# Optimization experiments

Hardware: AMD Instinct MI355X
Metric: run time of the kernel (lower is better)

## Reference

```python
import jax, jax.numpy as jnp
import numpy as np

T, D, H, HD = 2048, 2048, 16, 128
ROPE_BASE = 10000.0
NEG = jnp.float32(-1e30)


def rms_norm(x):
    # F.rms_norm(x, (x.size(-1),)) with default eps = dtype eps
    eps = jnp.finfo(x.dtype).eps
    return x * jax.lax.rsqrt(jnp.mean(x * x, axis=-1, keepdims=True) + eps)


def rotary(x):
    # x: [1, T, H, hd]; half-split rotation as in Rotary.forward
    hd = x.shape[-1]
    inv_freq = (1.0 / ROPE_BASE) ** (jnp.arange(0, hd, 2, dtype=jnp.float32) / hd)
    t = jnp.arange(x.shape[1], dtype=jnp.float32)
    freqs = jnp.outer(t, inv_freq)                      # [T, hd/2]
    cos = jnp.cos(freqs)[None, :, None, :]
    sin = jnp.sin(freqs)[None, :, None, :]
    x1, x2 = jnp.split(x, 2, axis=-1)
    return jnp.concatenate([x1 * cos + x2 * sin, -x1 * sin + x2 * cos], axis=-1)


def setup_inputs() -> dict:
    key = jax.random.key(0)
    ks = jax.random.split(key, 10)
    w = lambda k, shape: jax.random.normal(k, shape, jnp.float32) * 0.02
    return {
        "x":  jax.random.normal(ks[0], (1, T, D), jnp.float32),
        "vi": jax.random.normal(ks[1], (1, T, H, HD), jnp.float32),
        "x0": jax.random.normal(ks[2], (1, T, D), jnp.float32),
        "wq": w(ks[3], (D, D)),
        "wk": w(ks[4], (D, D)),
        "wv": w(ks[5], (D, D)),
        "wo": w(ks[6], (D, D)),
        "lamb": jnp.float32(0.5),
        "lambdas": jnp.array([1.0, 0.0], jnp.float32),
        "w_fc": w(ks[7], (4 * D, D)),
        "w_proj": w(ks[8], (D, 4 * D)),
    }


def reference(x, vi, x0, wq, wk, wv, wo, lamb, lambdas, w_fc, w_proj):
    # Block: residual blend with initial embedding x0
    xb = lambdas[0] * x + lambdas[1] * x0
    xn = rms_norm(xb)

    # --- CausalSelfAttention ---
    q = (xn @ wq.T).reshape(1, T, H, HD)
    k = (xn @ wk.T).reshape(1, T, H, HD)
    v = (xn @ wv.T).reshape(1, T, H, HD)
    v = (1.0 - lamb) * v + lamb * vi                     # value-embedding blend
    q = rotary(rms_norm(q))
    k = rotary(rms_norm(k))

    scale = 1.0 / jnp.sqrt(jnp.float32(HD))              # flex_attention default scale
    scores = jnp.einsum('bqhd,bkhd->bhqk', q, k) * scale # [1,H,T,T]
    causal = jnp.tril(jnp.ones((T, T), bool))
    scores = jnp.where(causal[None, None], scores, NEG)
    attn = jax.nn.softmax(scores, axis=-1)
    y = jnp.einsum('bhqk,bkhd->bqhd', attn, v).reshape(1, T, D)
    a = y @ wo.T                                         # attention output REPLACES x (no residual)

    # --- MLP with squared ReLU ---
    h = rms_norm(a) @ w_fc.T
    h = jnp.square(jax.nn.relu(h))
    out = a + h @ w_proj.T
    return out
```

## Files before the change

### kernel.cpp

```cpp
#include <hip/hip_runtime.h>
#include <hip/hip_bf16.h>

typedef __bf16 bf16;
typedef __bf16 bf16x8 __attribute__((ext_vector_type(8)));
typedef float f32x4 __attribute__((ext_vector_type(4)));
typedef unsigned int u32x4 __attribute__((ext_vector_type(4)));

#define DD 2048
#define DD2 4194304ull
#define G9_LDS 131072

__device__ __forceinline__ void glds16(const void* g, void* l) {
  __builtin_amdgcn_global_load_lds((const __attribute__((address_space(1))) void*)g,
                                   (__attribute__((address_space(3))) void*)l, 16, 0, 0);
}

__device__ __forceinline__ f32x4 mfma16(bf16x8 a, bf16x8 b, f32x4 c) {
  return __builtin_amdgcn_mfma_f32_16x16x32_bf16(a, b, c, 0, 0, 0);
}

__device__ __forceinline__ unsigned pk2(float lo, float hi) {
  unsigned short a = __builtin_bit_cast(unsigned short, (bf16)lo);
  unsigned short b = __builtin_bit_cast(unsigned short, (bf16)hi);
  return (unsigned)a | ((unsigned)b << 16);
}

__global__ __launch_bounds__(256) void cvt_seg(const float* __restrict__ s0, const float* __restrict__ s1,
                                               const float* __restrict__ s2, const float* __restrict__ s3,
                                               bf16* __restrict__ dst, int seglog, size_t total) {
  size_t i = ((size_t)blockIdx.x * 256 + threadIdx.x) * 16;
  const size_t stride = (size_t)gridDim.x * 256 * 16;
  for (; i < total; i += stride) {
    int seg = (int)(i >> seglog);
    const float* src = (seg == 0) ? s0 : (seg == 1) ? s1 : (seg == 2) ? s2 : s3;
    size_t loc = i - ((size_t)seg << seglog);
    float4 a0 = *(const float4*)(src + loc);
    float4 a1 = *(const float4*)(src + loc + 4);
    float4 a2 = *(const float4*)(src + loc + 8);
    float4 a3 = *(const float4*)(src + loc + 12);
    bf16x8 o0, o1;
    o0[0] = (bf16)a0.x; o0[1] = (bf16)a0.y; o0[2] = (bf16)a0.z; o0[3] = (bf16)a0.w;
    o0[4] = (bf16)a1.x; o0[5] = (bf16)a1.y; o0[6] = (bf16)a1.z; o0[7] = (bf16)a1.w;
    o1[0] = (bf16)a2.x; o1[1] = (bf16)a2.y; o1[2] = (bf16)a2.z; o1[3] = (bf16)a2.w;
    o1[4] = (bf16)a3.x; o1[5] = (bf16)a3.y; o1[6] = (bf16)a3.z; o1[7] = (bf16)a3.w;
    *(bf16x8*)(dst + i) = o0;
    *(bf16x8*)(dst + i + 8) = o1;
  }
}

template<bool BLEND>
__global__ __launch_bounds__(256) void prenorm_k(const float* __restrict__ x, const float* __restrict__ x0,
                                                 const float* __restrict__ lambdas, bf16* __restrict__ out) {
  const int t = blockIdx.x, tid = threadIdx.x;
  const float4* xr = (const float4*)(x + (size_t)t * DD);
  float4 a0 = xr[2 * tid], a1 = xr[2 * tid + 1];
  float v[8] = {a0.x, a0.y, a0.z, a0.w, a1.x, a1.y, a1.z, a1.w};
  if (BLEND) {
    const float l0 = lambdas[0], l1 = lambdas[1];
    const float4* yr = (const float4*)(x0 + (size_t)t * DD);
    float4 b0 = yr[2 * tid], b1 = yr[2 * tid + 1];
    float w[8] = {b0.x, b0.y, b0.z, b0.w, b1.x, b1.y, b1.z, b1.w};
#pragma unroll
    for (int i = 0; i < 8; ++i) v[i] = l0 * v[i] + l1 * w[i];
  }
  float ss = 0.f;
#pragma unroll
  for (int i = 0; i < 8; ++i) ss += v[i] * v[i];
#pragma unroll
  for (int off = 1; off < 64; off <<= 1) ss += __shfl_xor(ss, off, 64);
  __shared__ float red[4];
  const int wid = tid >> 6;
  if ((tid & 63) == 0) red[wid] = ss;
  __syncthreads();
  ss = red[0] + red[1] + red[2] + red[3];
  const float sc = rsqrtf(ss * (1.0f / DD) + 1.1920928955078125e-07f);
  bf16x8 o;
#pragma unroll
  for (int i = 0; i < 8; ++i) o[i] = (bf16)(v[i] * sc);
  *(bf16x8*)(out + (size_t)t * DD + tid * 8) = o;
}

__global__ __launch_bounds__(256) void rope_k(bf16* __restrict__ qg, bf16* __restrict__ kg) {
  const int tid = threadIdx.x, lane = tid & 63, wid = tid >> 6;
  const int p = blockIdx.x * 4 + wid;
  bf16* base = ((p >> 15) ? kg : qg);
  const int t = (p >> 4) & 2047, hh = p & 15;
  base += (size_t)t * DD + hh * 128;
  float x1 = (float)base[lane], x2 = (float)base[lane + 64];
  float ss = x1 * x1 + x2 * x2;
#pragma unroll
  for (int off = 1; off < 64; off <<= 1) ss += __shfl_xor(ss, off, 64);
  const float sc = rsqrtf(ss * (1.0f / 128.0f) + 1.1920928955078125e-07f);
  x1 *= sc; x2 *= sc;
  const float fr = (float)t * exp2f((float)lane * (-13.287712379549449f / 64.0f));
  const float s = sinf(fr), c = cosf(fr);
  base[lane]      = (bf16)(x1 * c + x2 * s);
  base[lane + 64] = (bf16)(-x1 * s + x2 * c);
}

__global__ __launch_bounds__(256) void vt_k(const bf16* __restrict__ v, bf16* __restrict__ vt) {
  __shared__ alignas(16) bf16 tile[16 * 128];
  const int tb = blockIdx.x, hb = blockIdx.y, tid = threadIdx.x;
  glds16(v + (size_t)(tb * 16 + (tid >> 4)) * DD + hb * 128 + (tid & 15) * 8, tile + tid * 8);
  __syncthreads();
  const int d_l = tid & 127, tc = tid >> 7;
  bf16x8 o;
#pragma unroll
  for (int i = 0; i < 8; ++i) o[i] = tile[(tc * 8 + i) * 128 + d_l];
  *(bf16x8*)(vt + (size_t)(hb * 128 + d_l) * DD + tb * 16 + tc * 8) = o;
}

__device__ __forceinline__ void g9_stageA(const bf16* A, int Kstride, int row0, int k0,
                                          bf16* buf, int hm, int tid) {
#pragma unroll
  for (int i = 0; i < 2; ++i) {
    int e = tid + i * 512;
    int prl = e >> 3, slot = e & 7;
    int wm = prl >> 6, r63 = prl & 63;
    glds16(A + (size_t)(row0 + wm * 128 + hm * 64 + r63) * Kstride + k0 + ((slot ^ (prl & 7)) * 8),
           buf + hm * 8192 + e * 8);
  }
}
__device__ __forceinline__ void g9_stageB(const bf16* B, int Kstride, int col0, int k0,
                                          bf16* buf, int hn, int tid) {
#pragma unroll
  for (int i = 0; i < 2; ++i) {
    int e = tid + i * 512;
    int pbl = e >> 3, slot = e & 7;
    int wn = pbl >> 5, q = pbl & 31;
    glds16(B + (size_t)(col0 + wn * 64 + hn * 32 + q) * Kstride + k0 + ((slot ^ (pbl & 7)) * 8),
           buf + 16384 + hn * 8192 + e * 8);
  }
}

__device__ __forceinline__ void gemm9_core(const bf16* __restrict__ A, const bf16* __restrict__ B,
                                           int Kstride, int Klen, int row0, int col0,
                                           bf16* smem, f32x4 (&acc)[8][4]) {
  const int tid = threadIdx.x, lane = tid & 63, wid = tid >> 6;
  const int wm = wid >> 2, wn = wid & 3;
  const int l15 = lane & 15, g = lane >> 4;
  const int sw = l15 & 7;
  const int NT = Klen >> 6;
  g9_stageA(A, Kstride, row0, 0, smem, 0, tid);
  g9_stageB(B, Kstride, col0, 0, smem, 0, tid);
  g9_stageB(B, Kstride, col0, 0, smem, 1, tid);
  g9_stageA(A, Kstride, row0, 0, smem, 1, tid);
  asm volatile("s_waitcnt vmcnt(4)" ::: "memory");
  __builtin_amdgcn_s_barrier();

  bf16x8 a[4][2], b0[2][2], b1[2][2];
  for (int t = 0; t < NT; ++t) {
    bf16* cb = smem + (t & 1) * 32768;
    bf16* sb = smem + ((t + 1) & 1) * 32768;
    const int ks0 = (t + 1) << 6;
    const bool st = (t + 1) < NT;
#pragma unroll
    for (int mm = 0; mm < 4; ++mm)
#pragma unroll
      for (int ks = 0; ks < 2; ++ks)
        a[mm][ks] = *(const bf16x8*)(cb + (wm * 64 + mm * 16 + l15) * 64 + (((ks * 4 + g) ^ sw) * 8));
#pragma unroll
    for (int nn = 0; nn < 2; ++nn)
#pragma unroll
      for (int ks = 0; ks < 2; ++ks)
        b0[nn][ks] = *(const bf16x8*)(cb + 16384 + (wn * 32 + nn * 16 + l15) * 64 + (((ks * 4 + g) ^ sw) * 8));
    if (st) g9_stageA(A, Kstride, row0, ks0, sb, 0, tid);
    if (st) { asm volatile("s_waitcnt vmcnt(4)" ::: "memory"); }
    else    { asm volatile("s_waitcnt vmcnt(2)" ::: "memory"); }
    __builtin_amdgcn_s_barrier();
    __builtin_amdgcn_s_setprio(1);
#pragma unroll
    for (int mm = 0; mm < 4; ++mm)
#pragma unroll
      for (int nn = 0; nn < 2; ++nn)
#pragma unroll
        for (int ks = 0; ks < 2; ++ks)
          acc[mm][nn] = mfma16(a[mm][ks], b0[nn][ks], acc[mm][nn]);
    __builtin_amdgcn_s_setprio(0);
#pragma unroll
    for (int nn = 0; nn < 2; ++nn)
#pragma unroll
      for (int ks = 0; ks < 2; ++ks)
        b1[nn][ks] = *(const bf16x8*)(cb + 16384 + 8192 + (wn * 32 + nn * 16 + l15) * 64 + (((ks * 4 + g) ^ sw) * 8));
    if (st) g9_stageB(B, Kstride, col0, ks0, sb, 0, tid);
    if (st) { asm volatile("s_waitcnt vmcnt(4)" ::: "memory"); }
    else    { asm volatile("s_waitcnt vmcnt(0)" ::: "memory"); }
    __builtin_amdgcn_s_barrier();
    __builtin_amdgcn_s_setprio(1);
#pragma unroll
    for (int mm = 0; mm < 4; ++mm)
#pragma unroll
      for (int nn = 0; nn < 2; ++nn)
#pragma unroll
        for (int ks = 0; ks < 2; ++ks)
          acc[mm][2 + nn] = mfma16(a[mm][ks], b1[nn][ks], acc[mm][2 + nn]);
    __builtin_amdgcn_s_setprio(0);
#pragma unroll
    for (int mm = 0; mm < 4; ++mm)
#pragma unroll
      for (int ks = 0; ks < 2; ++ks)
        a[mm][ks] = *(const bf16x8*)(cb + 8192 + (wm * 64 + mm * 16 + l15) * 64 + (((ks * 4 + g) ^ sw) * 8));
    if (st) g9_stageB(B, Kstride, col0, ks0, sb, 1, tid);
    __builtin_amdgcn_s_barrier();
    __builtin_amdgcn_s_setprio(1);
#pragma unroll
    for (int mm = 0; mm < 4; ++mm)
#pragma unroll
      for (int nn = 0; nn < 2; ++nn)
#pragma unroll
        for (int ks = 0; ks < 2; ++ks)
          acc[4 + mm][nn] = mfma16(a[mm][ks], b0[nn][ks], acc[4 + mm][nn]);
    __builtin_amdgcn_s_setprio(0);
    if (st) { g9_stageA(A, Kstride, row0, ks0, sb, 1, tid);
              asm volatile("s_waitcnt vmcnt(4)" ::: "memory"); }
    __builtin_amdgcn_s_barrier();
    __builtin_amdgcn_s_setprio(1);
#pragma unroll
    for (int mm = 0; mm < 4; ++mm)
#pragma unroll
      for (int nn = 0; nn < 2; ++nn)
#pragma unroll
        for (int ks = 0; ks < 2; ++ks)
          acc[4 + mm][2 + nn] = mfma16(a[mm][ks], b1[nn][ks], acc[4 + mm][2 + nn]);
    __builtin_amdgcn_s_setprio(0);
  }
}

#define GEMM9_EPI(STMT)                                                        \
  { const int lane_ = threadIdx.x & 63, wid_ = threadIdx.x >> 6;               \
    const int l15_ = lane_ & 15, g_ = lane_ >> 4;                              \
    const int wm_ = wid_ >> 2, wn_ = wid_ & 3;                                 \
    _Pragma("unroll") for (int m = 0; m < 8; ++m)                              \
    _Pragma("unroll") for (int n = 0; n < 4; ++n)                              \
    _Pragma("unroll") for (int j = 0; j < 4; ++j) {                            \
      int grow = row0 + wm_ * 128 + (m >> 2) * 64 + (m & 3) * 16 + g_ * 4 + j; \
      int gcol = col0 + wn_ * 64 + (n >> 1) * 32 + (n & 1) * 16 + l15_;        \
      float vacc = acc[m][n][j];                                               \
      STMT; } }

__global__ __launch_bounds__(512, 1) void gemm9_qkv(const bf16* __restrict__ A,
    const bf16* __restrict__ Wq, const bf16* __restrict__ Wk, const bf16* __restrict__ Wv,
    bf16* __restrict__ oq, bf16* __restrict__ ok, bf16* __restrict__ ov,
    const float* __restrict__ vi, const float* __restrict__ lambp) {
  extern __shared__ bf16 smem9[];
  const int z = blockIdx.z;
  const bf16* B = (z == 0) ? Wq : (z == 1) ? Wk : Wv;
  bf16* out = (z == 0) ? oq : (z == 1) ? ok : ov;
  const int row0 = blockIdx.y * 256, col0 = blockIdx.x * 256;
  f32x4 acc[8][4] = {};
  gemm9_core(A, B, DD, DD, row0, col0, smem9, acc);
  if (z < 2) {
    GEMM9_EPI( out[(size_t)grow * DD + gcol] = (bf16)vacc; )
  } else {
    const float lam = *lambp;
    GEMM9_EPI( out[(size_t)grow * DD + gcol] =
                 (bf16)((1.0f - lam) * vacc + lam * vi[(size_t)grow * DD + gcol]); )
  }
}

__global__ __launch_bounds__(512, 1) void gemm9_part(const bf16* __restrict__ A, const bf16* __restrict__ B,
                                                     float* __restrict__ o1, float* __restrict__ o2,
                                                     int zsw, int N, int Kstride, int Klen) {
  extern __shared__ bf16 smem9[];
  const int row0 = blockIdx.y * 256, col0 = blockIdx.x * 256;
  const int z = blockIdx.z, kofs = z * Klen;
  float* out = (z < zsw) ? (o1 + (size_t)z * DD2) : (o2 + (size_t)(z - zsw) * DD2);
  f32x4 acc[8][4] = {};
  gemm9_core(A + kofs, B + kofs, Kstride, Klen, row0, col0, smem9, acc);
  GEMM9_EPI( out[(size_t)grow * N + gcol] = vacc; )
}

__global__ __launch_bounds__(512, 1) void gemm9_relu(const bf16* __restrict__ A, const bf16* __restrict__ B,
                                                     bf16* __restrict__ out, int N, int Kstride, int Klen) {
  extern __shared__ bf16 smem9[];
  const int row0 = blockIdx.y * 256, col0 = blockIdx.x * 256;
  f32x4 acc[8][4] = {};
  gemm9_core(A, B, Kstride, Klen, row0, col0, smem9, acc);
  GEMM9_EPI( float r = fmaxf(vacc, 0.f); out[(size_t)grow * N + gcol] = (bf16)(r * r); )
}

__global__ __launch_bounds__(256) void wo_red_prenorm(const float* __restrict__ pa, const float* __restrict__ pb,
                                                      float* __restrict__ a_f, bf16* __restrict__ an) {
  const int t = blockIdx.x, tid = threadIdx.x;
  const size_t base = (size_t)t * DD + tid * 8;
  float v[8];
#pragma unroll
  for (int h = 0; h < 2; ++h) {
    size_t i = base + h * 4;
    float4 r0 = *(const float4*)(pa + i);
    float4 r1 = *(const float4*)(pa + DD2 + i);
    float4 r2 = *(const float4*)(pb + i);
    float4 r3 = *(const float4*)(pb + DD2 + i);
    v[h*4+0] = r0.x + r1.x + r2.x + r3.x;
    v[h*4+1] = r0.y + r1.y + r2.y + r3.y;
    v[h*4+2] = r0.z + r1.z + r2.z + r3.z;
    v[h*4+3] = r0.w + r1.w + r2.w + r3.w;
  }
  *(float4*)(a_f + base)     = make_float4(v[0], v[1], v[2], v[3]);
  *(float4*)(a_f + base + 4) = make_float4(v[4], v[5], v[6], v[7]);
  float ss = 0.f;
#pragma unroll
  for (int i = 0; i < 8; ++i) ss += v[i] * v[i];
#pragma unroll
  for (int off = 1; off < 64; off <<= 1) ss += __shfl_xor(ss, off, 64);
  __shared__ float red[4];
  if ((tid & 63) == 0) red[tid >> 6] = ss;
  __syncthreads();
  ss = red[0] + red[1] + red[2] + red[3];
  const float sc = rsqrtf(ss * (1.0f / DD) + 1.1920928955078125e-07f);
  bf16x8 o;
#pragma unroll
  for (int i = 0; i < 8; ++i) o[i] = (bf16)(v[i] * sc);
  *(bf16x8*)(an + base) = o;
}

__global__ __launch_bounds__(256) void proj_red(const float* __restrict__ pa, const float* __restrict__ pw,
                                                const float* __restrict__ a_f, float* __restrict__ out) {
  const size_t base = ((size_t)blockIdx.x * 256 + threadIdx.x) * 8;
#pragma unroll
  for (int h = 0; h < 2; ++h) {
    size_t i = base + h * 4;
    float4 r = *(const float4*)(a_f + i);
    float4 u = *(const float4*)(pa + i);
    float4 w = *(const float4*)(pa + DD2 + i);
    float4 z = *(const float4*)(pa + 2 * DD2 + i);
    float4 y = *(const float4*)(pw + i);
    *(float4*)(out + i) = make_float4(r.x + u.x + w.x + z.x + y.x,
                                      r.y + u.y + w.y + z.y + y.y,
                                      r.z + u.z + w.z + z.z + y.z,
                                      r.w + u.w + w.w + z.w + y.w);
  }
}

__device__ __forceinline__ void att_stageK(const bf16* kg, int h, int kt, bf16* dst, int tid) {
#pragma unroll
  for (int r = 0; r < 2; ++r) {
    int e = tid + r * 256, row = e >> 4, slot = e & 15;
    glds16(kg + (size_t)(kt * 32 + row) * DD + h * 128 + ((slot ^ (row & 7)) * 8), dst + e * 8);
  }
}
__device__ __forceinline__ void att_stageV(const bf16* vtg, int h, int kt, bf16* dst, int tid) {
#pragma unroll
  for (int r = 0; r < 2; ++r) {
    int e = tid + r * 256, d = e >> 2, slot = e & 3;
    glds16(vtg + (size_t)(h * 128 + d) * DD + kt * 32 + ((slot ^ ((d >> 1) & 3)) * 8), dst + e * 8);
  }
}

__global__ __launch_bounds__(256) void attn_k(const bf16* __restrict__ qg, const bf16* __restrict__ kg,
                                              const bf16* __restrict__ vtg, bf16* __restrict__ yg) {
  __shared__ alignas(16) bf16 Ks[3][32 * 128];
  __shared__ alignas(16) bf16 Vt[3][128 * 32];
  const int h = blockIdx.y, qb = 31 - blockIdx.x;
  const int tid = threadIdx.x, lane = tid & 63, wid = tid >> 6;
  const int l15 = lane & 15, g = lane >> 4, swl = l15 & 7;
  const int qrow = qb * 64 + wid * 16;
  const float scale = 0.08838834764831845f;
  bf16x8 aQ[4];
  {
    const bf16* qp = qg + (size_t)(qrow + l15) * DD + h * 128 + g * 8;
#pragma unroll
    for (int kc = 0; kc < 4; ++kc) aQ[kc] = *(const bf16x8*)(qp + kc * 32);
  }
  f32x4 acc[8] = {};
  float lsum = 0.f;
  const int nkt = qb * 2 + 2;
  att_stageK(kg, h, 0, Ks[0], tid);
  att_stageV(vtg, h, 0, Vt[0], tid);
  att_stageK(kg, h, 1, Ks[1], tid);
  att_stageV(vtg, h, 1, Vt[1], tid);
  asm volatile("s_waitcnt vmcnt(4)" ::: "memory");
  __builtin_amdgcn_s_barrier();
  int cur = 0;
  for (int kt = 0; kt < nkt; ++kt) {
    const int kbase = kt * 32;
    const int nb = (cur >= 1) ? cur - 1 : 2;
    bf16x8 kf0[4], kf1[4];
#pragma unroll
    for (int kc = 0; kc < 4; ++kc) {
      kf0[kc] = *(const bf16x8*)(Ks[cur] + l15 * 128 + (((kc * 4 + g) ^ swl) * 8));
      kf1[kc] = *(const bf16x8*)(Ks[cur] + (16 + l15) * 128 + (((kc * 4 + g) ^ swl) * 8));
    }
    if (kt + 2 < nkt) { att_stageK(kg, h, kt + 2, Ks[nb], tid);
                        att_stageV(vtg, h, kt + 2, Vt[nb], tid); }
    f32x4 S0 = {}, S1 = {};
#pragma unroll
    for (int kc = 0; kc < 4; ++kc) {
      S0 = mfma16(kf0[kc], aQ[kc], S0);
      S1 = mfma16(kf1[kc], aQ[kc], S1);
    }
    const int q = qrow + l15;
    float p0[4], p1[4];
#pragma unroll
    for (int j = 0; j < 4; ++j) {
      int k0 = kbase + 4 * g + j;
      p0[j] = (k0 <= q) ? __expf(S0[j] * scale) : 0.f;
      p1[j] = (k0 + 16 <= q) ? __expf(S1[j] * scale) : 0.f;
      lsum += p0[j] + p1[j];
    }
    unsigned w0 = pk2(p0[0], p0[1]), w1 = pk2(p0[2], p0[3]);
    unsigned w2 = pk2(p1[0], p1[1]), w3 = pk2(p1[2], p1[3]);
    const int s0l = (g & 1) * 32 + l15, s1l = s0l + 16;
    const bool hi = g >= 2;
    unsigned t00 = __shfl(w0, s0l, 64), t10 = __shfl(w1, s0l, 64);
    unsigned t01 = __shfl(w0, s1l, 64), t11 = __shfl(w1, s1l, 64);
    unsigned u00 = __shfl(w2, s0l, 64), u10 = __shfl(w3, s0l, 64);
    unsigned u01 = __shfl(w2, s1l, 64), u11 = __shfl(w3, s1l, 64);
    u32x4 av = { hi ? u00 : t00, hi ? u10 : t10, hi ? u01 : t01, hi ? u11 : t11 };
    bf16x8 aP = __builtin_bit_cast(bf16x8, av);
#pragma unroll
    for (int dt = 0; dt < 8; ++dt) {
      int d = dt * 16 + l15;
      bf16x8 bV = *(const bf16x8*)(Vt[cur] + d * 32 + ((g ^ ((d >> 1) & 3)) * 8));
      acc[dt] = mfma16(aP, bV, acc[dt]);
    }
    if (kt + 1 < nkt) {
      if (kt + 2 < nkt) { asm volatile("s_waitcnt vmcnt(4)" ::: "memory"); }
      else              { asm volatile("s_waitcnt vmcnt(0)" ::: "memory"); }
      __builtin_amdgcn_s_barrier();
    }
    cur = (cur == 2) ? 0 : cur + 1;
  }
  lsum += __shfl_xor(lsum, 16, 64);
  lsum += __shfl_xor(lsum, 32, 64);
  f32x4 linv;
#pragma unroll
  for (int j = 0; j < 4; ++j) linv[j] = 1.0f / __shfl(lsum, 4 * g + j, 64);
#pragma unroll
  for (int dt = 0; dt < 8; ++dt)
#pragma unroll
    for (int j = 0; j < 4; ++j) {
      int q = qrow + 4 * g + j;
      yg[(size_t)q * DD + h * 128 + dt * 16 + l15] = (bf16)(acc[dt][j] * linv[j]);
    }
}

extern "C" void kernel_launch(void* const* d_in, const int* in_sizes, int n_in,
                              void* d_out, int out_size, void* d_ws, size_t ws_size,
                              hipStream_t stream) {
  const float* x       = (const float*)d_in[0];
  const float* vi      = (const float*)d_in[1];
  const float* x0      = (const float*)d_in[2];
  const float* wq      = (const float*)d_in[3];
  const float* wk      = (const float*)d_in[4];
  const float* wv      = (const float*)d_in[5];
  const float* wo      = (const float*)d_in[6];
  const float* lamb    = (const float*)d_in[7];
  const float* lambdas = (const float*)d_in[8];
  const float* wfc     = (const float*)d_in[9];
  const float* wproj   = (const float*)d_in[10];
  float* out = (float*)d_out;

  (void)hipFuncSetAttribute(reinterpret_cast<const void*>(gemm9_qkv),
                            hipFuncAttributeMaxDynamicSharedMemorySize, G9_LDS);
  (void)hipFuncSetAttribute(reinterpret_cast<const void*>(gemm9_part),
                            hipFuncAttributeMaxDynamicSharedMemorySize, G9_LDS);
  (void)hipFuncSetAttribute(reinterpret_cast<const void*>(gemm9_relu),
                            hipFuncAttributeMaxDynamicSharedMemorySize, G9_LDS);

  char* wsb = (char*)d_ws;
  size_t off = 0;
  auto alloc = [&](size_t bytes) { void* p = wsb + off; off = (off + bytes + 255) & ~(size_t)255; return p; };
  bf16* wq_b  = (bf16*)alloc(DD2 * 2);
  bf16* wk_b  = (bf16*)alloc(DD2 * 2);
  bf16* wv_b  = (bf16*)alloc(DD2 * 2);
  bf16* wo_b  = (bf16*)alloc(DD2 * 2);
  bf16* wfc_b = (bf16*)alloc(DD2 * 8);
  bf16* wpj_b = (bf16*)alloc(DD2 * 8);
  bf16* xn_b  = (bf16*)alloc(DD2 * 2);
  bf16* q_b   = (bf16*)alloc(DD2 * 2);
  bf16* k_b   = (bf16*)alloc(DD2 * 2);
  bf16* v_b   = (bf16*)alloc(DD2 * 2);
  bf16* y_b   = (bf16*)alloc(DD2 * 2);
  bf16* an_b  = (bf16*)alloc(DD2 * 2);
  float* partA = (float*)xn_b;
  float* a_f  = (float*)alloc(DD2 * 4);
  bf16* h_b   = (bf16*)alloc(DD2 * 8);
  bf16* vt_b  = h_b;
  float* partB = (float*)h_b;

  cvt_seg<<<2048, 256, 0, stream>>>(wq, wk, wv, wo, (bf16*)wsb, 22, 4 * DD2);
  prenorm_k<true><<<2048, 256, 0, stream>>>(x, x0, lambdas, xn_b);
  gemm9_qkv<<<dim3(8, 8, 3), 512, G9_LDS, stream>>>(xn_b, wq_b, wk_b, wv_b, q_b, k_b, v_b, vi, lamb);
  rope_k<<<16384, 256, 0, stream>>>(q_b, k_b);
  vt_k<<<dim3(128, 16), 256, 0, stream>>>(v_b, vt_b);
  attn_k<<<dim3(32, 16), 256, 0, stream>>>(q_b, k_b, vt_b, y_b);
  gemm9_part<<<dim3(8, 8, 4), 512, G9_LDS, stream>>>(y_b, wo_b, partA, partB, 2, DD, DD, 512);
  wo_red_prenorm<<<2048, 256, 0, stream>>>(partA, partB, a_f, an_b);
  cvt_seg<<<2048, 256, 0, stream>>>(wfc, wproj, wfc, wfc, wfc_b, 24, 8 * DD2);
  gemm9_relu<<<dim3(32, 8), 512, G9_LDS, stream>>>(an_b, wfc_b, h_b, 4 * DD, DD, DD);
  gemm9_part<<<dim3(8, 8, 4), 512, G9_LDS, stream>>>(h_b, wpj_b, partA, (float*)wfc_b, 3, DD, 4 * DD, 2048);
  proj_red<<<2048, 256, 0, stream>>>(partA, (float*)wfc_b, a_f, out);
}
```

Before: 386.0 us.

## Shrink GEMM tiles to 128x128 and halve split-K partitions

Replaces the 256x256-tile GEMM core (128 KB LDS, one block per CU) with a 128x128-tile core using 64 KB LDS and launch bounds allowing several blocks per CU. Grids grow accordingly, and split-K for the output and projection GEMMs drops from four partitions to two, so the reduction kernels read fewer partial buffers. The aim is more resident blocks and less partial-sum traffic. The cost is lower arithmetic intensity per tile, more global and LDS traffic per FLOP, and longer K loops per block.

After: 387.5 us. Within noise of the previous version (+0.4%).

```diff
diff --git a/kernel.cpp b/kernel.cpp
--- a/kernel.cpp
+++ b/kernel.cpp
@@ -8,7 +8,7 @@
 
 #define DD 2048
 #define DD2 4194304ull
-#define G9_LDS 131072
+#define G10_LDS 65536
 
 __device__ __forceinline__ void glds16(const void* g, void* l) {
   __builtin_amdgcn_global_load_lds((const __attribute__((address_space(1))) void*)g,
@@ -110,176 +110,162 @@
   *(bf16x8*)(vt + (size_t)(hb * 128 + d_l) * DD + tb * 16 + tc * 8) = o;
 }
 
-__device__ __forceinline__ void g9_stageA(const bf16* A, int Kstride, int row0, int k0,
-                                          bf16* buf, int hm, int tid) {
-#pragma unroll
-  for (int i = 0; i < 2; ++i) {
-    int e = tid + i * 512;
-    int prl = e >> 3, slot = e & 7;
-    int wm = prl >> 6, r63 = prl & 63;
-    glds16(A + (size_t)(row0 + wm * 128 + hm * 64 + r63) * Kstride + k0 + ((slot ^ (prl & 7)) * 8),
-           buf + hm * 8192 + e * 8);
-  }
-}
-__device__ __forceinline__ void g9_stageB(const bf16* B, int Kstride, int col0, int k0,
-                                          bf16* buf, int hn, int tid) {
-#pragma unroll
-  for (int i = 0; i < 2; ++i) {
-    int e = tid + i * 512;
-    int pbl = e >> 3, slot = e & 7;
-    int wn = pbl >> 5, q = pbl & 31;
-    glds16(B + (size_t)(col0 + wn * 64 + hn * 32 + q) * Kstride + k0 + ((slot ^ (pbl & 7)) * 8),
-           buf + 16384 + hn * 8192 + e * 8);
-  }
-}
-
-__device__ __forceinline__ void gemm9_core(const bf16* __restrict__ A, const bf16* __restrict__ B,
-                                           int Kstride, int Klen, int row0, int col0,
-                                           bf16* smem, f32x4 (&acc)[8][4]) {
+__device__ __forceinline__ void g10_stageA(const bf16* A, int Kstride, int row0, int k0,
+                                           bf16* buf, int hm, int tid) {
+  int prl = tid >> 3, slot = tid & 7;
+  int wmb = prl >> 5, r31 = prl & 31;
+  glds16(A + (size_t)(row0 + wmb * 64 + hm * 32 + r31) * Kstride + k0 + ((slot ^ (prl & 7)) * 8),
+         buf + hm * 4096 + tid * 8);
+}
+__device__ __forceinline__ void g10_stageB(const bf16* B, int Kstride, int col0, int k0,
+                                           bf16* buf, int hn, int tid) {
+  int pbl = tid >> 3, slot = tid & 7;
+  int wnb = pbl >> 4, c15 = pbl & 15;
+  glds16(B + (size_t)(col0 + wnb * 32 + hn * 16 + c15) * Kstride + k0 + ((slot ^ (pbl & 7)) * 8),
+         buf + 8192 + hn * 4096 + tid * 8);
+}
+
+__device__ __forceinline__ void gemm10_core(const bf16* __restrict__ A, const bf16* __restrict__ B,
+                                            int Kstride, int Klen, int row0, int col0,
+                                            bf16* smem, f32x4 (&acc)[4][2]) {
   const int tid = threadIdx.x, lane = tid & 63, wid = tid >> 6;
   const int wm = wid >> 2, wn = wid & 3;
   const int l15 = lane & 15, g = lane >> 4;
-  const int sw = l15 & 7;
   const int NT = Klen >> 6;
-  g9_stageA(A, Kstride, row0, 0, smem, 0, tid);
-  g9_stageB(B, Kstride, col0, 0, smem, 0, tid);
-  g9_stageB(B, Kstride, col0, 0, smem, 1, tid);
-  g9_stageA(A, Kstride, row0, 0, smem, 1, tid);
-  asm volatile("s_waitcnt vmcnt(4)" ::: "memory");
+  g10_stageA(A, Kstride, row0, 0, smem, 0, tid);
+  g10_stageB(B, Kstride, col0, 0, smem, 0, tid);
+  g10_stageB(B, Kstride, col0, 0, smem, 1, tid);
+  g10_stageA(A, Kstride, row0, 0, smem, 1, tid);
+  asm volatile("s_waitcnt vmcnt(2)" ::: "memory");
   __builtin_amdgcn_s_barrier();
 
-  bf16x8 a[4][2], b0[2][2], b1[2][2];
+  bf16x8 a[2][2], b0[2], b1[2];
   for (int t = 0; t < NT; ++t) {
-    bf16* cb = smem + (t & 1) * 32768;
-    bf16* sb = smem + ((t + 1) & 1) * 32768;
-    const int ks0 = (t + 1) << 6;
+    bf16* cb = smem + (t & 1) * 16384;
+    bf16* nb = smem + ((t + 1) & 1) * 16384;
+    const int kst = (t + 1) << 6;
     const bool st = (t + 1) < NT;
 #pragma unroll
-    for (int mm = 0; mm < 4; ++mm)
-#pragma unroll
-      for (int ks = 0; ks < 2; ++ks)
-        a[mm][ks] = *(const bf16x8*)(cb + (wm * 64 + mm * 16 + l15) * 64 + (((ks * 4 + g) ^ sw) * 8));
-#pragma unroll
-    for (int nn = 0; nn < 2; ++nn)
-#pragma unroll
-      for (int ks = 0; ks < 2; ++ks)
-        b0[nn][ks] = *(const bf16x8*)(cb + 16384 + (wn * 32 + nn * 16 + l15) * 64 + (((ks * 4 + g) ^ sw) * 8));
-    if (st) g9_stageA(A, Kstride, row0, ks0, sb, 0, tid);
-    if (st) { asm volatile("s_waitcnt vmcnt(4)" ::: "memory"); }
-    else    { asm volatile("s_waitcnt vmcnt(2)" ::: "memory"); }
+    for (int mm = 0; mm < 2; ++mm)
+#pragma unroll
+      for (int ks = 0; ks < 2; ++ks) {
+        int pr = wm * 32 + mm * 16 + l15;
+        a[mm][ks] = *(const bf16x8*)(cb + pr * 64 + (((ks * 4 + g) ^ (pr & 7)) * 8));
+      }
+#pragma unroll
+    for (int ks = 0; ks < 2; ++ks) {
+      int pb = wn * 16 + l15;
+      b0[ks] = *(const bf16x8*)(cb + 8192 + pb * 64 + (((ks * 4 + g) ^ (pb & 7)) * 8));
+    }
+    if (st) { g10_stageA(A, Kstride, row0, kst, nb, 0, tid);
+              asm volatile("s_waitcnt vmcnt(2)" ::: "memory"); }
+    else    { asm volatile("s_waitcnt vmcnt(1)" ::: "memory"); }
     __builtin_amdgcn_s_barrier();
     __builtin_amdgcn_s_setprio(1);
 #pragma unroll
-    for (int mm = 0; mm < 4; ++mm)
-#pragma unroll
-      for (int nn = 0; nn < 2; ++nn)
-#pragma unroll
-        for (int ks = 0; ks < 2; ++ks)
-          acc[mm][nn] = mfma16(a[mm][ks], b0[nn][ks], acc[mm][nn]);
+    for (int mm = 0; mm < 2; ++mm)
+#pragma unroll
+      for (int ks = 0; ks < 2; ++ks)
+        acc[mm][0] = mfma16(a[mm][ks], b0[ks], acc[mm][0]);
     __builtin_amdgcn_s_setprio(0);
 #pragma unroll
-    for (int nn = 0; nn < 2; ++nn)
-#pragma unroll
-      for (int ks = 0; ks < 2; ++ks)
-        b1[nn][ks] = *(const bf16x8*)(cb + 16384 + 8192 + (wn * 32 + nn * 16 + l15) * 64 + (((ks * 4 + g) ^ sw) * 8));
-    if (st) g9_stageB(B, Kstride, col0, ks0, sb, 0, tid);
-    if (st) { asm volatile("s_waitcnt vmcnt(4)" ::: "memory"); }
+    for (int ks = 0; ks < 2; ++ks) {
+      int pb = wn * 16 + l15;
+      b1[ks] = *(const bf16x8*)(cb + 8192 + 4096 + pb * 64 + (((ks * 4 + g) ^ (pb & 7)) * 8));
+    }
+    if (st) { g10_stageB(B, Kstride, col0, kst, nb, 0, tid);
+              asm volatile("s_waitcnt vmcnt(2)" ::: "memory"); }
     else    { asm volatile("s_waitcnt vmcnt(0)" ::: "memory"); }
     __builtin_amdgcn_s_barrier();
     __builtin_amdgcn_s_setprio(1);
 #pragma unroll
-    for (int mm = 0; mm < 4; ++mm)
-#pragma unroll
-      for (int nn = 0; nn < 2; ++nn)
-#pragma unroll
-        for (int ks = 0; ks < 2; ++ks)
-          acc[mm][2 + nn] = mfma16(a[mm][ks], b1[nn][ks], acc[mm][2 + nn]);
+    for (int mm = 0; mm < 2; ++mm)
+#pragma unroll
+      for (int ks = 0; ks < 2; ++ks)
+        acc[mm][1] = mfma16(a[mm][ks], b1[ks], acc[mm][1]);
     __builtin_amdgcn_s_setprio(0);
 #pragma unroll
-    for (int mm = 0; mm < 4; ++mm)
-#pragma unroll
-      for (int ks = 0; ks < 2; ++ks)
-        a[mm][ks] = *(const bf16x8*)(cb + 8192 + (wm * 64 + mm * 16 + l15) * 64 + (((ks * 4 + g) ^ sw) * 8));
-    if (st) g9_stageB(B, Kstride, col0, ks0, sb, 1, tid);
+    for (int mm = 0; mm < 2; ++mm)
+#pragma unroll
+      for (int ks = 0; ks < 2; ++ks) {
+        int pr = 64 + wm * 32 + mm * 16 + l15;
+        a[mm][ks] = *(const bf16x8*)(cb + pr * 64 + (((ks * 4 + g) ^ (pr & 7)) * 8));
+      }
+    if (st) g10_stageB(B, Kstride, col0, kst, nb, 1, tid);
     __builtin_amdgcn_s_barrier();
     __builtin_amdgcn_s_setprio(1);
 #pragma unroll
-    for (int mm = 0; mm < 4; ++mm)
-#pragma unroll
-      for (int nn = 0; nn < 2; ++nn)
-#pragma unroll
-        for (int ks = 0; ks < 2; ++ks)
-          acc[4 + mm][nn] = mfma16(a[mm][ks], b0[nn][ks], acc[4 + mm][nn]);
+    for (int mm = 0; mm < 2; ++mm)
+#pragma unroll
+      for (int ks = 0; ks < 2; ++ks)
+        acc[2 + mm][0] = mfma16(a[mm][ks], b0[ks], acc[2 + mm][0]);
     __builtin_amdgcn_s_setprio(0);
-    if (st) { g9_stageA(A, Kstride, row0, ks0, sb, 1, tid);
-              asm volatile("s_waitcnt vmcnt(4)" ::: "memory"); }
+    if (st) { g10_stageA(A, Kstride, row0, kst, nb, 1, tid);
+              asm volatile("s_waitcnt vmcnt(2)" ::: "memory"); }
     __builtin_amdgcn_s_barrier();
     __builtin_amdgcn_s_setprio(1);
 #pragma unroll
-    for (int mm = 0; mm < 4; ++mm)
-#pragma unroll
-      for (int nn = 0; nn < 2; ++nn)
-#pragma unroll
-        for (int ks = 0; ks < 2; ++ks)
-          acc[4 + mm][2 + nn] = mfma16(a[mm][ks], b1[nn][ks], acc[4 + mm][2 + nn]);
+    for (int mm = 0; mm < 2; ++mm)
+#pragma unroll
+      for (int ks = 0; ks < 2; ++ks)
+        acc[2 + mm][1] = mfma16(a[mm][ks], b1[ks], acc[2 + mm][1]);
     __builtin_amdgcn_s_setprio(0);
   }
 }
 
-#define GEMM9_EPI(STMT)                                                        \
+#define GEMM10_EPI(STMT)                                                       \
   { const int lane_ = threadIdx.x & 63, wid_ = threadIdx.x >> 6;               \
     const int l15_ = lane_ & 15, g_ = lane_ >> 4;                              \
     const int wm_ = wid_ >> 2, wn_ = wid_ & 3;                                 \
-    _Pragma("unroll") for (int m = 0; m < 8; ++m)                              \
-    _Pragma("unroll") for (int n = 0; n < 4; ++n)                              \
+    _Pragma("unroll") for (int m = 0; m < 4; ++m)                              \
+    _Pragma("unroll") for (int n = 0; n < 2; ++n)                              \
     _Pragma("unroll") for (int j = 0; j < 4; ++j) {                            \
-      int grow = row0 + wm_ * 128 + (m >> 2) * 64 + (m & 3) * 16 + g_ * 4 + j; \
-      int gcol = col0 + wn_ * 64 + (n >> 1) * 32 + (n & 1) * 16 + l15_;        \
+      int grow = row0 + wm_ * 64 + (m >> 1) * 32 + (m & 1) * 16 + g_ * 4 + j;  \
+      int gcol = col0 + wn_ * 32 + n * 16 + l15_;                              \
       float vacc = acc[m][n][j];                                               \
       STMT; } }
 
-__global__ __launch_bounds__(512, 1) void gemm9_qkv(const bf16* __restrict__ A,
+__global__ __launch_bounds__(512, 4) void gemm10_qkv(const bf16* __restrict__ A,
     const bf16* __restrict__ Wq, const bf16* __restrict__ Wk, const bf16* __restrict__ Wv,
     bf16* __restrict__ oq, bf16* __restrict__ ok, bf16* __restrict__ ov,
     const float* __restrict__ vi, const float* __restrict__ lambp) {
-  extern __shared__ bf16 smem9[];
+  extern __shared__ bf16 smem10[];
   const int z = blockIdx.z;
   const bf16* B = (z == 0) ? Wq : (z == 1) ? Wk : Wv;
   bf16* out = (z == 0) ? oq : (z == 1) ? ok : ov;
-  const int row0 = blockIdx.y * 256, col0 = blockIdx.x * 256;
-  f32x4 acc[8][4] = {};
-  gemm9_core(A, B, DD, DD, row0, col0, smem9, acc);
+  const int row0 = blockIdx.y * 128, col0 = blockIdx.x * 128;
+  f32x4 acc[4][2] = {};
+  gemm10_core(A, B, DD, DD, row0, col0, smem10, acc);
   if (z < 2) {
-    GEMM9_EPI( out[(size_t)grow * DD + gcol] = (bf16)vacc; )
+    GEMM10_EPI( out[(size_t)grow * DD + gcol] = (bf16)vacc; )
   } else {
     const float lam = *lambp;
-    GEMM9_EPI( out[(size_t)grow * DD + gcol] =
-                 (bf16)((1.0f - lam) * vacc + lam * vi[(size_t)grow * DD + gcol]); )
-  }
-}
-
-__global__ __launch_bounds__(512, 1) void gemm9_part(const bf16* __restrict__ A, const bf16* __restrict__ B,
-                                                     float* __restrict__ o1, float* __restrict__ o2,
-                                                     int zsw, int N, int Kstride, int Klen) {
-  extern __shared__ bf16 smem9[];
-  const int row0 = blockIdx.y * 256, col0 = blockIdx.x * 256;
-  const int z = blockIdx.z, kofs = z * Klen;
-  float* out = (z < zsw) ? (o1 + (size_t)z * DD2) : (o2 + (size_t)(z - zsw) * DD2);
-  f32x4 acc[8][4] = {};
-  gemm9_core(A + kofs, B + kofs, Kstride, Klen, row0, col0, smem9, acc);
-  GEMM9_EPI( out[(size_t)grow * N + gcol] = vacc; )
-}
-
-__global__ __launch_bounds__(512, 1) void gemm9_relu(const bf16* __restrict__ A, const bf16* __restrict__ B,
-                                                     bf16* __restrict__ out, int N, int Kstride, int Klen) {
-  extern __shared__ bf16 smem9[];
-  const int row0 = blockIdx.y * 256, col0 = blockIdx.x * 256;
-  f32x4 acc[8][4] = {};
-  gemm9_core(A, B, Kstride, Klen, row0, col0, smem9, acc);
-  GEMM9_EPI( float r = fmaxf(vacc, 0.f); out[(size_t)grow * N + gcol] = (bf16)(r * r); )
-}
-
-__global__ __launch_bounds__(256) void wo_red_prenorm(const float* __restrict__ pa, const float* __restrict__ pb,
+    GEMM10_EPI( out[(size_t)grow * DD + gcol] =
+                  (bf16)((1.0f - lam) * vacc + lam * vi[(size_t)grow * DD + gcol]); )
+  }
+}
+
+__global__ __launch_bounds__(512, 4) void gemm10_part(const bf16* __restrict__ A, const bf16* __restrict__ B,
+                                                      float* __restrict__ o1, int N, int Kstride, int Klen) {
+  extern __shared__ bf16 smem10[];
+  const int row0 = blockIdx.y * 128, col0 = blockIdx.x * 128;
+  const int kofs = blockIdx.z * Klen;
+  float* out = o1 + (size_t)blockIdx.z * DD2;
+  f32x4 acc[4][2] = {};
+  gemm10_core(A + kofs, B + kofs, Kstride, Klen, row0, col0, smem10, acc);
+  GEMM10_EPI( out[(size_t)grow * N + gcol] = vacc; )
+}
+
+__global__ __launch_bounds__(512, 4) void gemm10_relu(const bf16* __restrict__ A, const bf16* __restrict__ B,
+                                                      bf16* __restrict__ out, int N, int Kstride, int Klen) {
+  extern __shared__ bf16 smem10[];
+  const int row0 = blockIdx.y * 128, col0 = blockIdx.x * 128;
+  f32x4 acc[4][2] = {};
+  gemm10_core(A, B, Kstride, Klen, row0, col0, smem10, acc);
+  GEMM10_EPI( float r = fmaxf(vacc, 0.f); out[(size_t)grow * N + gcol] = (bf16)(r * r); )
+}
+
+__global__ __launch_bounds__(256) void wo_red_prenorm(const float* __restrict__ pa,
                                                       float* __restrict__ a_f, bf16* __restrict__ an) {
   const int t = blockIdx.x, tid = threadIdx.x;
   const size_t base = (size_t)t * DD + tid * 8;
@@ -289,12 +275,10 @@
     size_t i = base + h * 4;
     float4 r0 = *(const float4*)(pa + i);
     float4 r1 = *(const float4*)(pa + DD2 + i);
-    float4 r2 = *(const float4*)(pb + i);
-    float4 r3 = *(const float4*)(pb + DD2 + i);
-    v[h*4+0] = r0.x + r1.x + r2.x + r3.x;
-    v[h*4+1] = r0.y + r1.y + r2.y + r3.y;
-    v[h*4+2] = r0.z + r1.z + r2.z + r3.z;
-    v[h*4+3] = r0.w + r1.w + r2.w + r3.w;
+    v[h*4+0] = r0.x + r1.x;
+    v[h*4+1] = r0.y + r1.y;
+    v[h*4+2] = r0.z + r1.z;
+    v[h*4+3] = r0.w + r1.w;
   }
   *(float4*)(a_f + base)     = make_float4(v[0], v[1], v[2], v[3]);
   *(float4*)(a_f + base + 4) = make_float4(v[4], v[5], v[6], v[7]);
@@ -314,7 +298,7 @@
   *(bf16x8*)(an + base) = o;
 }
 
-__global__ __launch_bounds__(256) void proj_red(const float* __restrict__ pa, const float* __restrict__ pw,
+__global__ __launch_bounds__(256) void proj_red(const float* __restrict__ pa,
                                                 const float* __restrict__ a_f, float* __restrict__ out) {
   const size_t base = ((size_t)blockIdx.x * 256 + threadIdx.x) * 8;
 #pragma unroll
@@ -323,12 +307,8 @@
     float4 r = *(const float4*)(a_f + i);
     float4 u = *(const float4*)(pa + i);
     float4 w = *(const float4*)(pa + DD2 + i);
-    float4 z = *(const float4*)(pa + 2 * DD2 + i);
-    float4 y = *(const float4*)(pw + i);
-    *(float4*)(out + i) = make_float4(r.x + u.x + w.x + z.x + y.x,
-                                      r.y + u.y + w.y + z.y + y.y,
-                                      r.z + u.z + w.z + z.z + y.z,
-                                      r.w + u.w + w.w + z.w + y.w);
+    *(float4*)(out + i) = make_float4(r.x + u.x + w.x, r.y + u.y + w.y,
+                                      r.z + u.z + w.z, r.w + u.w + w.w);
   }
 }
 
@@ -451,12 +431,12 @@
   const float* wproj   = (const float*)d_in[10];
   float* out = (float*)d_out;
 
-  (void)hipFuncSetAttribute(reinterpret_cast<const void*>(gemm9_qkv),
-                            hipFuncAttributeMaxDynamicSharedMemorySize, G9_LDS);
-  (void)hipFuncSetAttribute(reinterpret_cast<const void*>(gemm9_part),
-                            hipFuncAttributeMaxDynamicSharedMemorySize, G9_LDS);
-  (void)hipFuncSetAttribute(reinterpret_cast<const void*>(gemm9_relu),
-                            hipFuncAttributeMaxDynamicSharedMemorySize, G9_LDS);
+  (void)hipFuncSetAttribute(reinterpret_cast<const void*>(gemm10_qkv),
+                            hipFuncAttributeMaxDynamicSharedMemorySize, G10_LDS);
+  (void)hipFuncSetAttribute(reinterpret_cast<const void*>(gemm10_part),
+                            hipFuncAttributeMaxDynamicSharedMemorySize, G10_LDS);
+  (void)hipFuncSetAttribute(reinterpret_cast<const void*>(gemm10_relu),
+                            hipFuncAttributeMaxDynamicSharedMemorySize, G10_LDS);
 
   char* wsb = (char*)d_ws;
   size_t off = 0;
@@ -477,18 +457,17 @@
   float* a_f  = (float*)alloc(DD2 * 4);
   bf16* h_b   = (bf16*)alloc(DD2 * 8);
   bf16* vt_b  = h_b;
-  float* partB = (float*)h_b;
 
   cvt_seg<<<2048, 256, 0, stream>>>(wq, wk, wv, wo, (bf16*)wsb, 22, 4 * DD2);
   prenorm_k<true><<<2048, 256, 0, stream>>>(x, x0, lambdas, xn_b);
-  gemm9_qkv<<<dim3(8, 8, 3), 512, G9_LDS, stream>>>(xn_b, wq_b, wk_b, wv_b, q_b, k_b, v_b, vi, lamb);
+  gemm10_qkv<<<dim3(16, 16, 3), 512, G10_LDS, stream>>>(xn_b, wq_b, wk_b, wv_b, q_b, k_b, v_b, vi, lamb);
   rope_k<<<16384, 256, 0, stream>>>(q_b, k_b);
   vt_k<<<dim3(128, 16), 256, 0, stream>>>(v_b, vt_b);
   attn_k<<<dim3(32, 16), 256, 0, stream>>>(q_b, k_b, vt_b, y_b);
-  gemm9_part<<<dim3(8, 8, 4), 512, G9_LDS, stream>>>(y_b, wo_b, partA, partB, 2, DD, DD, 512);
-  wo_red_prenorm<<<2048, 256, 0, stream>>>(partA, partB, a_f, an_b);
+  gemm10_part<<<dim3(16, 16, 2), 512, G10_LDS, stream>>>(y_b, wo_b, partA, DD, DD, 1024);
+  wo_red_prenorm<<<2048, 256, 0, stream>>>(partA, a_f, an_b);
   cvt_seg<<<2048, 256, 0, stream>>>(wfc, wproj, wfc, wfc, wfc_b, 24, 8 * DD2);
-  gemm9_relu<<<dim3(32, 8), 512, G9_LDS, stream>>>(an_b, wfc_b, h_b, 4 * DD, DD, DD);
-  gemm9_part<<<dim3(8, 8, 4), 512, G9_LDS, stream>>>(h_b, wpj_b, partA, (float*)wfc_b, 3, DD, 4 * DD, 2048);
-  proj_red<<<2048, 256, 0, stream>>>(partA, (float*)wfc_b, a_f, out);
-}
+  gemm10_relu<<<dim3(64, 16), 512, G10_LDS, stream>>>(an_b, wfc_b, h_b, 4 * DD, DD, DD);
+  gemm10_part<<<dim3(16, 16, 2), 512, G10_LDS, stream>>>(h_b, wpj_b, partA, DD, 4 * DD, 4096);
+  proj_red<<<2048, 256, 0, stream>>>(partA, a_f, out);
+}
```
